# Performance work log

Measured on AMD Instinct MI355X. Metric: run time of the kernel, lower is better.

The kernel has to match this reference:

```python
import jax, jax.numpy as jnp
import numpy as np

H, W = 56, 56
N = H * W
C = 2
THETA_ALPHA = 160.0
THETA_BETA = 3.0
THETA_GAMMA = 3.0
NUM_ITERATIONS = 10


def setup_inputs() -> dict:
    key = jax.random.key(0)
    k1, k2, k3, k4 = jax.random.split(key, 4)
    inputs = jax.random.uniform(k1, (2, H, W), dtype=jnp.float32)
    # Keras 'uniform' initializer: U(-0.05, 0.05)
    sp_w = jax.random.uniform(k2, (C, C), minval=-0.05, maxval=0.05, dtype=jnp.float32)
    bl_w = jax.random.uniform(k3, (C, C), minval=-0.05, maxval=0.05, dtype=jnp.float32)
    compat = jax.random.uniform(k4, (C, C), minval=-0.05, maxval=0.05, dtype=jnp.float32)
    return {"inputs": inputs, "spatial_ker_weights": sp_w,
            "bilateral_ker_weights": bl_w, "compatibility_matrix": compat}


def _sqdist(f):
    # f: [N, D] -> [N, N] squared pairwise distances
    s = jnp.sum(f * f, axis=1)
    return s[:, None] + s[None, :] - 2.0 * (f @ f.T)


def _kernels(rgb_flat):
    # rgb_flat: [N, 3] pixel colors (0..255)
    ys, xs = jnp.meshgrid(jnp.arange(H, dtype=jnp.float32),
                          jnp.arange(W, dtype=jnp.float32), indexing="ij")
    pos = jnp.stack([xs.reshape(-1), ys.reshape(-1)], axis=1)  # [N, 2]
    # spatial (Gaussian) kernel: exp(-||p-q||^2 / (2*gamma^2))
    k_sp = jnp.exp(-0.5 * _sqdist(pos / THETA_GAMMA))
    # bilateral kernel: positions scaled by alpha, colors by beta
    f_bl = jnp.concatenate([pos / THETA_ALPHA, rgb_flat / THETA_BETA], axis=1)
    k_bl = jnp.exp(-0.5 * _sqdist(f_bl))
    return k_sp, k_bl


def reference(inputs, spatial_ker_weights, bilateral_ker_weights, compatibility_matrix):
    unary = inputs[0]            # [H, W], foreground prob
    gray = inputs[1] * 255.0     # [H, W], image intensities scaled as in the layer

    # unaries: [C, H, W] with channel 0 = 1-u, channel 1 = u
    unaries = jnp.stack([1.0 - unary, unary], axis=0).reshape(C, N)

    rgb_flat = jnp.tile(gray.reshape(-1)[:, None], (1, 3))  # [N, 3]

    k_sp, k_bl = _kernels(rgb_flat)
    ones = jnp.ones((N,), dtype=jnp.float32)
    norm_sp = k_sp @ ones  # [N]
    norm_bl = k_bl @ ones  # [N]

    q = unaries
    for i in range(NUM_ITERATIONS):
        softmax_out = q if i == 0 else jax.nn.softmax(q, axis=0)
        spatial_out = (softmax_out @ k_sp) / norm_sp[None, :]     # [C, N]
        bilateral_out = (softmax_out @ k_bl) / norm_bl[None, :]   # [C, N]
        message = spatial_ker_weights @ spatial_out + bilateral_ker_weights @ bilateral_out
        pairwise = compatibility_matrix @ message                 # [C, N]
        q = unaries - pairwise

    cur_q = q.reshape(C, H, W).transpose(1, 2, 0)  # [H, W, C]
    obj_prob = jax.nn.softmax(cur_q, axis=2)[:, :, 1]
    return obj_prob.reshape(1, H, W)
```

## Files before the change

kernel.cpp:

```cpp
#include <hip/hip_runtime.h>


namespace {

constexpr int NPIX = 3136;
constexpr int WIMG = 56;
constexpr int JPB  = 16;
constexpr int NBLK = NPIX / JPB;
constexpr int NTHR = 512;
constexpr int NQ   = NPIX / 4;
constexpr int NBUF = 9;
constexpr int Q2   = NQ - NTHR;
constexpr int NBIN = 128;
constexpr int BANDB = 9;
constexpr int NCHK = 98;
constexpr int CPX  = 32;

constexpr float LOG2E = 1.4426950408889634f;
constexpr float C1 = -LOG2E / 18.0f;
constexpr float C2 = -LOG2E / 51200.0f;
constexpr float C3 = -LOG2E / 6.0f;

constexpr int O_SSH  = 0;
constexpr int O_GSRT = 12544;
constexpr int O_MSRT = 25088;
constexpr int O_OFF  = 31360;
constexpr int O_WSX  = 31888;
constexpr int O_WSY  = 35472;
constexpr int O_LIDX = 39056;
constexpr int POOLSZ = 42192;

#define REDUCE32(v) \
    { v += __shfl_xor(v, 1); v += __shfl_xor(v, 2); v += __shfl_xor(v, 4); \
      v += __shfl_xor(v, 8); v += __shfl_xor(v, 16); }
#define REDUCE64(v) \
    { v += __shfl_xor(v, 1); v += __shfl_xor(v, 2); v += __shfl_xor(v, 4); \
      v += __shfl_xor(v, 8); v += __shfl_xor(v, 16); v += __shfl_xor(v, 32); }

__global__ __launch_bounds__(NTHR) void crf_all(
    const float* __restrict__ inp,
    const float* __restrict__ spw, const float* __restrict__ blw,
    const float* __restrict__ cmw,
    float* sbufs, float* __restrict__ out)
{
    __shared__ __align__(16) unsigned char pool[POOLSZ];
    float*  s_sh  = (float*)(pool + O_SSH);
    float4* s_sh4 = (float4*)(pool + O_SSH);
    float*  g_srt = (float*)(pool + O_GSRT);
    unsigned short* m_srt = (unsigned short*)(pool + O_MSRT);
    unsigned*       offs  = (unsigned*)(pool + O_OFF);
    float*  wsx   = (float*)(pool + O_WSX);
    float*  wsy   = (float*)(pool + O_WSY);
    unsigned char*  lidx = (unsigned char*)(pool + O_LIDX);
    unsigned short* H  = (unsigned short*)(pool + O_SSH);
    unsigned*       Hz = (unsigned*)(pool + O_SSH);

    const int t   = threadIdx.x;
    const int bid = blockIdx.x;
    const int sub = t & 31;
    const int jl  = t >> 5;
    const int j   = bid * JPB + jl;
    const int xj  = j % WIMG;
    const int yj  = j / WIMG;
    const float xjf = (float)xj, yjf = (float)yj;

    const float uj = inp[j];
    const float gj = inp[NPIX + j] * 255.0f;

    const float e0 = cmw[2] - cmw[0];
    const float e1 = cmw[3] - cmw[1];
    const float alpha = e0 * (spw[0] + blw[0]) + e1 * (spw[2] + blw[2]);
    const float beta  = e0 * (spw[1] - spw[0]) + e1 * (spw[3] - spw[2]);
    const float gamma = e0 * (blw[1] - blw[0]) + e1 * (blw[3] - blw[2]);

    for (int i = t; i < 6272; i += NTHR) Hz[i] = 0u;
    for (int idx = t; idx < JPB * 56; idx += NTHR) {
        const int jlw = idx / 56, p = idx - jlw * 56;
        const int jj = bid * JPB + jlw;
        const float ddx = (float)(jj % WIMG - p);
        const float ddy = (float)(jj / WIMG - p);
        wsx[idx] = __builtin_amdgcn_exp2f(C1 * ddx * ddx);
        wsy[idx] = __builtin_amdgcn_exp2f(C1 * ddy * ddy);
    }
    __syncthreads();
    if (t < NCHK) {
        unsigned short* Hr = H + t * NBIN;
        const int mb = t * CPX;
        for (int i = 0; i < CPX; ++i) {
            int b = (int)(inp[NPIX + mb + i] * 255.0f);
            b = (b > 255 ? 255 : b) >> 1;
            lidx[mb + i] = (unsigned char)Hr[b];
            Hr[b] = (unsigned short)(Hr[b] + 1);
        }
    }
    __syncthreads();
    if (t < NBIN) {
        unsigned run = 0;
        for (int c = 0; c < NCHK; ++c) {
            unsigned short v = H[c * NBIN + t];
            H[c * NBIN + t] = (unsigned short)run;
            run += v;
        }
        offs[t] = run;
    }
    __syncthreads();
    if (t < 64) {
        unsigned v0 = offs[2 * t], v1 = offs[2 * t + 1];
        unsigned sum = v0 + v1;
        unsigned sc = sum;
        for (int d = 1; d < 64; d <<= 1) {
            unsigned n = __shfl_up(sc, d);
            if (t >= d) sc += n;
        }
        unsigned base = sc - sum;
        offs[2 * t] = base;
        offs[2 * t + 1] = base + v0;
        if (t == 63) offs[NBIN] = sc;
    }
    __syncthreads();
    for (int m = t; m < NPIX; m += NTHR) {
        int b = (int)(inp[NPIX + m] * 255.0f);
        b = (b > 255 ? 255 : b) >> 1;
        const int r = (int)offs[b] + (int)H[(m >> 5) * NBIN + b] + (int)lidx[m];
        m_srt[r] = (unsigned short)m;
    }
    __syncthreads();
    for (int p = t; p < NPIX; p += NTHR)
        g_srt[p] = inp[NPIX + (int)m_srt[p]] * 255.0f;
    {
        const float4* u4 = (const float4*)inp;
        for (int q = t; q < NQ; q += NTHR) s_sh4[q] = u4[q];
    }
    __syncthreads();

    float sx, sy;
    {
        float dd = xjf - (float)sub;
        sx = __builtin_amdgcn_exp2f(C1 * dd * dd);
        if (sub + 32 < 56) {
            float d2 = xjf - (float)(sub + 32);
            sx += __builtin_amdgcn_exp2f(C1 * d2 * d2);
        }
        REDUCE32(sx);
        dd = yjf - (float)sub;
        sy = __builtin_amdgcn_exp2f(C1 * dd * dd);
        if (sub + 32 < 56) {
            float d2 = yjf - (float)(sub + 32);
            sy += __builtin_amdgcn_exp2f(C1 * d2 * d2);
        }
        REDUCE32(sy);
    }
    const float rnsp = 1.0f / (sx * sy);

    int bj = (int)gj; bj = (bj > 255 ? 255 : bj) >> 1;
    const int b0 = bj < BANDB ? 0 : bj - BANDB;
    const int b1 = bj + BANDB > NBIN - 1 ? NBIN - 1 : bj + BANDB;
    const int blo = (int)offs[b0];
    const int bhi = (int)offs[b1 + 1];

    auto spatial = [&]() -> float {
        const int wv = t >> 6;
        const int ln = t & 63;
        float v0 = 0.f, v1 = 0.f;
        if (ln < 56) {
            const float4* S = s_sh4 + ln * 14;
            float4 sv[14];
#pragma unroll
            for (int q = 0; q < 14; ++q) sv[q] = S[q];
            const int c0 = wv * 2, c1 = c0 + 1;
            const float4* R0 = (const float4*)(wsx + c0 * 56);
            const float4* R1 = (const float4*)(wsx + c1 * 56);
            float a0 = 0.f, a1 = 0.f;
#pragma unroll
            for (int q = 0; q < 14; ++q) {
                float4 w0 = R0[q], w1 = R1[q];
                a0 = fmaf(w0.x, sv[q].x, a0); a0 = fmaf(w0.y, sv[q].y, a0);
                a0 = fmaf(w0.z, sv[q].z, a0); a0 = fmaf(w0.w, sv[q].w, a0);
                a1 = fmaf(w1.x, sv[q].x, a1); a1 = fmaf(w1.y, sv[q].y, a1);
                a1 = fmaf(w1.z, sv[q].z, a1); a1 = fmaf(w1.w, sv[q].w, a1);
            }
            v0 = wsy[c0 * 56 + ln] * a0;
            v1 = wsy[c1 * 56 + ln] * a1;
        }
        REDUCE64(v0); REDUCE64(v1);
        return (ln < 32) ? v0 : v1;
    };

    auto bilateral = [&](float* nacc_out) -> float {
        float acc = 0.f, nacc = 0.f;
        int p = blo + sub;
#define BIL_BODY(MM, GG, SS) { \
            const int yi = (MM * 9363) >> 19; \
            const int xi = MM - yi * 56; \
            const float ux = (float)xi - xjf, vy = (float)yi - yjf; \
            const float r2 = fmaf(ux, ux, vy * vy); \
            const float dg = GG - gj; \
            const float w = __builtin_amdgcn_exp2f(fmaf(dg * C3, dg, r2 * C2)); \
            acc = fmaf(w, SS, acc); \
            if (nacc_out) nacc += w; }
        for (; p + 96 < bhi; p += 128) {
            const int m0 = m_srt[p],      m1 = m_srt[p + 32];
            const int m2 = m_srt[p + 64], m3 = m_srt[p + 96];
            const float g0 = g_srt[p],      g1 = g_srt[p + 32];
            const float g2 = g_srt[p + 64], g3 = g_srt[p + 96];
            const float s0 = s_sh[m0], s1 = s_sh[m1];
            const float s2 = s_sh[m2], s3 = s_sh[m3];
            BIL_BODY(m0, g0, s0) BIL_BODY(m1, g1, s1)
            BIL_BODY(m2, g2, s2) BIL_BODY(m3, g3, s3)
        }
        for (; p < bhi; p += 32) {
            const int mm = (int)m_srt[p];
            const float gg = g_srt[p];
            const float ss = s_sh[mm];
            BIL_BODY(mm, gg, ss)
        }
#undef BIL_BODY
        REDUCE32(acc);
        if (nacc_out) { REDUCE32(nacc); *nacc_out = nacc; }
        return acc;
    };

    auto publish_sync = [&](float s, float* buf) {
        if (sub == 0)
            __hip_atomic_store(&buf[j], s, __ATOMIC_RELAXED,
                               __HIP_MEMORY_SCOPE_AGENT);
        const float4* src = (const float4*)buf;
        float4 a, b;
        const bool two = (t < Q2);
        bool da = false, db = !two;
        for (;;) {
            if (!da)
                asm volatile("global_load_dwordx4 %0, %1, off sc0 sc1"
                             : "=&v"(a) : "v"(src + t));
            if (!db)
                asm volatile("global_load_dwordx4 %0, %1, off sc0 sc1"
                             : "=&v"(b) : "v"(src + NTHR + t));
            asm volatile("s_waitcnt vmcnt(0)" ::: "memory");
            if (!da) da = (fminf(fminf(a.x, a.y), fminf(a.z, a.w)) != 0.0f);
            if (!db) db = (fminf(fminf(b.x, b.y), fminf(b.z, b.w)) != 0.0f);
            if (da && db) break;
        }
        s_sh4[t] = a;
        if (two) s_sh4[NTHR + t] = b;
        __syncthreads();
    };

    const float base = 2.0f * uj - 1.0f - alpha;
    float rnbl, s;

    {
        float tsp = spatial();
        float nacc;
        float acc = bilateral(&nacc);
        rnbl = 1.0f / nacc;
        float d = base - beta * (tsp * rnsp) - gamma * (acc * rnbl);
        s = 1.0f / (1.0f + __builtin_amdgcn_exp2f(-d * LOG2E));
    }
    publish_sync(s, sbufs);

    for (int k = 1; k < 10; ++k) {
        float tsp = spatial();
        float acc = bilateral(nullptr);
        float d = base - beta * (tsp * rnsp) - gamma * (acc * rnbl);
        s = 1.0f / (1.0f + __builtin_amdgcn_exp2f(-d * LOG2E));
        if (k < 9) publish_sync(s, sbufs + k * NPIX);
        else if (sub == 0) out[j] = s;
    }
}

}

extern "C" void kernel_launch(void* const* d_in, const int* in_sizes, int n_in,
                              void* d_out, int out_size, void* d_ws, size_t ws_size,
                              hipStream_t stream) {
    const float* inp = (const float*)d_in[0];
    const float* spw = (const float*)d_in[1];
    const float* blw = (const float*)d_in[2];
    const float* cmw = (const float*)d_in[3];
    float* sbufs = (float*)d_ws;
    float* out = (float*)d_out;

    hipMemsetAsync(sbufs, 0, NBUF * NPIX * sizeof(float), stream);
    crf_all<<<dim3(NBLK), dim3(NTHR), 0, stream>>>(inp, spw, blw, cmw,
                                                   sbufs, out);
}
```

Before: 63.72 us.

## Store softmax values and coordinates in intensity-sorted order for bilateral loop

Blocks now publish their softmax values into the global exchange buffer at their intensity-sorted rank, and each block keeps both sorted and unsorted copies of the state in shared memory. Sorted arrays for state and packed x/y coordinates let the bilateral inner loop read contiguous shared memory instead of gathering through the sorted index array and decoding pixel coordinates with integer math. This removes indirect LDS reads from the hot loop. In exchange it adds a scatter into the unsorted copy after every sync and uses more shared memory, about 67 KB instead of 42 KB.

Measured after the change: 76.42 us. 1.2x slower.

```diff
diff --git a/kernel.cpp b/kernel.cpp
--- a/kernel.cpp
+++ b/kernel.cpp
@@ -22,13 +22,15 @@
 constexpr float C3 = -LOG2E / 6.0f;
 
 constexpr int O_SSH  = 0;
-constexpr int O_GSRT = 12544;
-constexpr int O_MSRT = 25088;
-constexpr int O_OFF  = 31360;
-constexpr int O_WSX  = 31888;
-constexpr int O_WSY  = 35472;
-constexpr int O_LIDX = 39056;
-constexpr int POOLSZ = 42192;
+constexpr int O_SSRT = 12544;
+constexpr int O_GSRT = 25088;
+constexpr int O_XYV  = 37632;
+constexpr int O_MSRT = 50176;
+constexpr int O_OFF  = 56448;
+constexpr int O_WSX  = 56976;
+constexpr int O_WSY  = 60560;
+constexpr int O_LIDX = 64144;
+constexpr int POOLSZ = 67280;
 
 #define REDUCE32(v) \
     { v += __shfl_xor(v, 1); v += __shfl_xor(v, 2); v += __shfl_xor(v, 4); \
@@ -46,7 +48,10 @@
     __shared__ __align__(16) unsigned char pool[POOLSZ];
     float*  s_sh  = (float*)(pool + O_SSH);
     float4* s_sh4 = (float4*)(pool + O_SSH);
+    float*  s_srt = (float*)(pool + O_SSRT);
+    float4* s_srt4= (float4*)(pool + O_SSRT);
     float*  g_srt = (float*)(pool + O_GSRT);
+    float*  xyv_srt = (float*)(pool + O_XYV);
     unsigned short* m_srt = (unsigned short*)(pool + O_MSRT);
     unsigned*       offs  = (unsigned*)(pool + O_OFF);
     float*  wsx   = (float*)(pool + O_WSX);
@@ -124,9 +129,21 @@
         const int r = (int)offs[b] + (int)H[(m >> 5) * NBIN + b] + (int)lidx[m];
         m_srt[r] = (unsigned short)m;
     }
-    __syncthreads();
-    for (int p = t; p < NPIX; p += NTHR)
-        g_srt[p] = inp[NPIX + (int)m_srt[p]] * 255.0f;
+    int rank_j;
+    {
+        int b = (int)gj;
+        b = (b > 255 ? 255 : b) >> 1;
+        rank_j = (int)offs[b] + (int)H[(j >> 5) * NBIN + b] + (int)lidx[j];
+    }
+    __syncthreads();
+    for (int p = t; p < NPIX; p += NTHR) {
+        const int m = (int)m_srt[p];
+        s_srt[p] = inp[m];
+        g_srt[p] = inp[NPIX + m] * 255.0f;
+        const int yi = (m * 9363) >> 19;
+        const int xi = m - yi * 56;
+        xyv_srt[p] = (float)(xi + 64 * yi);
+    }
     {
         const float4* u4 = (const float4*)inp;
         for (int q = t; q < NQ; q += NTHR) s_sh4[q] = u4[q];
@@ -188,33 +205,20 @@
 
     auto bilateral = [&](float* nacc_out) -> float {
         float acc = 0.f, nacc = 0.f;
-        int p = blo + sub;
-#define BIL_BODY(MM, GG, SS) { \
-            const int yi = (MM * 9363) >> 19; \
-            const int xi = MM - yi * 56; \
-            const float ux = (float)xi - xjf, vy = (float)yi - yjf; \
-            const float r2 = fmaf(ux, ux, vy * vy); \
-            const float dg = GG - gj; \
-            const float w = __builtin_amdgcn_exp2f(fmaf(dg * C3, dg, r2 * C2)); \
-            acc = fmaf(w, SS, acc); \
-            if (nacc_out) nacc += w; }
-        for (; p + 96 < bhi; p += 128) {
-            const int m0 = m_srt[p],      m1 = m_srt[p + 32];
-            const int m2 = m_srt[p + 64], m3 = m_srt[p + 96];
-            const float g0 = g_srt[p],      g1 = g_srt[p + 32];
-            const float g2 = g_srt[p + 64], g3 = g_srt[p + 96];
-            const float s0 = s_sh[m0], s1 = s_sh[m1];
-            const float s2 = s_sh[m2], s3 = s_sh[m3];
-            BIL_BODY(m0, g0, s0) BIL_BODY(m1, g1, s1)
-            BIL_BODY(m2, g2, s2) BIL_BODY(m3, g3, s3)
-        }
-        for (; p < bhi; p += 32) {
-            const int mm = (int)m_srt[p];
-            const float gg = g_srt[p];
-            const float ss = s_sh[mm];
-            BIL_BODY(mm, gg, ss)
-        }
-#undef BIL_BODY
+#pragma unroll 2
+        for (int p = blo + sub; p < bhi; p += 32) {
+            const float xyv = xyv_srt[p];
+            const float gv  = g_srt[p];
+            const float sv  = s_srt[p];
+            const float yi  = floorf(xyv * 0.015625f);
+            const float xi  = fmaf(-64.f, yi, xyv);
+            const float ux = xi - xjf, vy = yi - yjf;
+            const float r2 = fmaf(ux, ux, vy * vy);
+            const float dg = gv - gj;
+            const float w = __builtin_amdgcn_exp2f(fmaf(dg * C3, dg, r2 * C2));
+            acc = fmaf(w, sv, acc);
+            if (nacc_out) nacc += w;
+        }
         REDUCE32(acc);
         if (nacc_out) { REDUCE32(nacc); *nacc_out = nacc; }
         return acc;
@@ -222,7 +226,7 @@
 
     auto publish_sync = [&](float s, float* buf) {
         if (sub == 0)
-            __hip_atomic_store(&buf[j], s, __ATOMIC_RELAXED,
+            __hip_atomic_store(&buf[rank_j], s, __ATOMIC_RELAXED,
                                __HIP_MEMORY_SCOPE_AGENT);
         const float4* src = (const float4*)buf;
         float4 a, b;
@@ -240,8 +244,22 @@
             if (!db) db = (fminf(fminf(b.x, b.y), fminf(b.z, b.w)) != 0.0f);
             if (da && db) break;
         }
-        s_sh4[t] = a;
-        if (two) s_sh4[NTHR + t] = b;
+        s_srt4[t] = a;
+        {
+            const int p4 = 4 * t;
+            s_sh[m_srt[p4 + 0]] = a.x;
+            s_sh[m_srt[p4 + 1]] = a.y;
+            s_sh[m_srt[p4 + 2]] = a.z;
+            s_sh[m_srt[p4 + 3]] = a.w;
+        }
+        if (two) {
+            s_srt4[NTHR + t] = b;
+            const int p4 = 4 * (NTHR + t);
+            s_sh[m_srt[p4 + 0]] = b.x;
+            s_sh[m_srt[p4 + 1]] = b.y;
+            s_sh[m_srt[p4 + 2]] = b.z;
+            s_sh[m_srt[p4 + 3]] = b.w;
+        }
         __syncthreads();
     };
 
```
